# Kernel tuning notes

Hardware: AMD Instinct MI355X
Metric: run time of the kernel (lower is better)

## Reference

```python
import jax, jax.numpy as jnp
import numpy as np

FP8_MAX = 448.0  # max representable magnitude of float8_e4m3fn


def act_quant(x, block_size):
    """Blockwise fp8 quantization along the last dim.
    x: [M, K] -> q: [M, K//bs, bs] fp8, scale: [M, K//bs, 1] fp32."""
    m, k = x.shape
    xb = x.reshape(m, k // block_size, block_size)
    amax = jnp.max(jnp.abs(xb), axis=-1, keepdims=True)
    scale = jnp.maximum(amax, 1e-4) / FP8_MAX
    q = (xb / scale).astype(jnp.float8_e4m3fn)
    return q, scale


def dequant(q, scale):
    # q: [M, K//bs, bs], scale: [M, K//bs, 1] -> [M, K] fp32
    return (q.astype(jnp.float32) * scale).reshape(q.shape[0], -1)


def setup_inputs() -> dict:
    key = jax.random.key(0)
    k1, k2 = jax.random.split(key)
    B, S, D, F = 16, 4096, 512, 512
    x = jax.random.normal(k1, (B, S, D), dtype=jnp.float32)
    # lecun_normal-style init: std = 1/sqrt(fan_in)
    kernel = jax.random.normal(k2, (D, F), dtype=jnp.float32) / np.sqrt(D)
    bias = jnp.zeros((F,), dtype=jnp.float32)
    return {"x": x, "kernel": kernel, "bias": bias, "block_size": 128}


def reference(x, kernel, bias, block_size):
    input_shape = x.shape
    x_flat = x.reshape(-1, input_shape[-1])  # [M, K]
    # blockwise fp8 quantize activations and kernel
    xq, xs = act_quant(x_flat, block_size)
    kq, ks = act_quant(kernel, block_size)
    # fp8 GEMM with dequant scales == dequant-then-matmul in exact math
    y = dequant(xq, xs) @ dequant(kq, ks)  # [M, F]
    y = y + bias
    return y.reshape(input_shape[:-1] + (kernel.shape[1],))
```

## Files before the change

### kernel.cpp

```cpp
#include <hip/hip_runtime.h>
#include <hip/hip_bf16.h>

typedef __attribute__((ext_vector_type(4))) float  floatx4;
typedef __attribute__((ext_vector_type(2))) float  floatx2;
typedef __attribute__((ext_vector_type(8))) __bf16 bf16x8;

#define FP8_MAX 448.0f

__device__ __forceinline__ floatx2 fp8_qdq2(float a, float b) {
    int p = __builtin_amdgcn_cvt_pk_fp8_f32(a, b, 0, false);
    return __builtin_amdgcn_cvt_pk_f32_fp8(p, false);
}

__device__ __forceinline__ unsigned int f2bf(float f) {
    union { __hip_bfloat16 h; unsigned short u; } cv;
    cv.h = __float2bfloat16(f);
    return (unsigned int)cv.u;
}

__device__ __forceinline__ void async_copy16(void* lds, const void* g) {
    __builtin_amdgcn_global_load_lds(
        (const __attribute__((address_space(1))) unsigned int*)g,
        (__attribute__((address_space(3))) unsigned int*)lds,
        16, 0, 0);
}

__global__ void wdq_kernel(const float* __restrict__ W,
                           __hip_bfloat16* __restrict__ Wt) {
    const int D = 512, F = 512;
    int d = blockIdx.x;
    int t = threadIdx.x;
    float4 v = *reinterpret_cast<const float4*>(W + (size_t)d * F + t * 4);
    float am = fmaxf(fmaxf(fabsf(v.x), fabsf(v.y)), fmaxf(fabsf(v.z), fabsf(v.w)));
#pragma unroll
    for (int s = 16; s >= 1; s >>= 1) am = fmaxf(am, __shfl_xor(am, s));
    float scale = fmaxf(am, 1e-4f) / FP8_MAX;
    floatx2 d01 = fp8_qdq2(v.x / scale, v.y / scale);
    floatx2 d23 = fp8_qdq2(v.z / scale, v.w / scale);
    int f0 = t * 4;
    Wt[(size_t)(f0 + 0) * D + d] = __float2bfloat16(d01[0] * scale);
    Wt[(size_t)(f0 + 1) * D + d] = __float2bfloat16(d01[1] * scale);
    Wt[(size_t)(f0 + 2) * D + d] = __float2bfloat16(d23[0] * scale);
    Wt[(size_t)(f0 + 3) * D + d] = __float2bfloat16(d23[1] * scale);
}

#define BM 64
#define BN 256
#define BK 128

__global__ __launch_bounds__(256, 3) void fused_gemm(
        const float* __restrict__ X,
        const __hip_bfloat16* __restrict__ Wt,
        const float* __restrict__ bias,
        float* __restrict__ C, int M) {
    const int K = 512, N = 512;
    __shared__ __hip_bfloat16 As[BM][BK];
    __shared__ __hip_bfloat16 Bs[BN][64];

    int bx   = blockIdx.x;
    int tN   = bx & 1;
    int tM   = bx >> 1;
    int tid  = threadIdx.x;
    int wid  = tid >> 6;
    int lane = tid & 63;

    const float* Xb = X + (size_t)tM * BM * K;
    const __hip_bfloat16* Wb = Wt + (size_t)tN * BN * K;

    int ar = tid >> 2;
    int aq = tid & 3;

    floatx4 acc[4][4] = {};

    for (int kt = 0; kt < K / BK; ++kt) {
        const int k0 = kt * BK;

#pragma unroll
        for (int c = 0; c < 8; ++c) {
            int chunk = wid * 8 + c;
            int frow  = chunk * 8 + (lane >> 3);
            async_copy16((char*)&Bs[0][0] + chunk * 1024,
                         (const char*)(Wb + (size_t)frow * K + k0) + (lane & 7) * 16);
        }

        float4 v[8];
        const float* src = Xb + (size_t)ar * K + k0 + aq * 32;
#pragma unroll
        for (int j = 0; j < 8; ++j)
            v[j] = *reinterpret_cast<const float4*>(src + j * 4);
        float am = 0.f;
#pragma unroll
        for (int j = 0; j < 8; ++j)
            am = fmaxf(am, fmaxf(fmaxf(fabsf(v[j].x), fabsf(v[j].y)),
                                 fmaxf(fabsf(v[j].z), fabsf(v[j].w))));
        am = fmaxf(am, __shfl_xor(am, 1));
        am = fmaxf(am, __shfl_xor(am, 2));
        am = fmaxf(am, 1e-4f);
        float scale = am / FP8_MAX;
        float inv   = FP8_MAX / am;
        unsigned int* dst = (unsigned int*)&As[ar][aq * 32];
#pragma unroll
        for (int j = 0; j < 4; ++j) {
            floatx2 a0 = fp8_qdq2(v[2*j].x   * inv, v[2*j].y   * inv);
            floatx2 a1 = fp8_qdq2(v[2*j].z   * inv, v[2*j].w   * inv);
            floatx2 a2 = fp8_qdq2(v[2*j+1].x * inv, v[2*j+1].y * inv);
            floatx2 a3 = fp8_qdq2(v[2*j+1].z * inv, v[2*j+1].w * inv);
            uint4 o;
            o.x = f2bf(a0[0] * scale) | (f2bf(a0[1] * scale) << 16);
            o.y = f2bf(a1[0] * scale) | (f2bf(a1[1] * scale) << 16);
            o.z = f2bf(a2[0] * scale) | (f2bf(a2[1] * scale) << 16);
            o.w = f2bf(a3[0] * scale) | (f2bf(a3[1] * scale) << 16);
            *reinterpret_cast<uint4*>(dst + j * 4) = o;
        }
        __syncthreads();

#pragma unroll
        for (int h = 0; h < 2; ++h) {
            if (h) {
#pragma unroll
                for (int c = 0; c < 8; ++c) {
                    int chunk = wid * 8 + c;
                    int frow  = chunk * 8 + (lane >> 3);
                    async_copy16((char*)&Bs[0][0] + chunk * 1024,
                                 (const char*)(Wb + (size_t)frow * K + k0 + 64) + (lane & 7) * 16);
                }
                __syncthreads();
            }
#pragma unroll
            for (int ks = 0; ks < 2; ++ks) {
                int ksg = h * 2 + ks;
                bf16x8 a[4], b[4];
#pragma unroll
                for (int i = 0; i < 4; ++i) {
                    a[i] = *reinterpret_cast<const bf16x8*>(
                        &As[i * 16 + (lane & 15)][ksg * 32 + (lane >> 4) * 8]);
                    b[i] = *reinterpret_cast<const bf16x8*>(
                        &Bs[wid * 64 + i * 16 + (lane & 15)][ks * 32 + (lane >> 4) * 8]);
                }
#pragma unroll
                for (int mi = 0; mi < 4; ++mi)
#pragma unroll
                    for (int ni = 0; ni < 4; ++ni)
                        acc[mi][ni] = __builtin_amdgcn_mfma_f32_16x16x32_bf16(
                            a[mi], b[ni], acc[mi][ni], 0, 0, 0);
            }
            __syncthreads();
        }
    }

    int fcol = tN * BN + wid * 64 + (lane & 15);
    int mrow = tM * BM + ((lane >> 4) << 2);
#pragma unroll
    for (int ni = 0; ni < 4; ++ni) {
        int f = fcol + ni * 16;
        float bv = bias[f];
#pragma unroll
        for (int mi = 0; mi < 4; ++mi) {
            int m0 = mrow + mi * 16;
#pragma unroll
            for (int e = 0; e < 4; ++e)
                C[(size_t)(m0 + e) * N + f] = acc[mi][ni][e] + bv;
        }
    }
}

extern "C" void kernel_launch(void* const* d_in, const int* in_sizes, int n_in,
                              void* d_out, int out_size, void* d_ws, size_t ws_size,
                              hipStream_t stream) {
    const float* X    = (const float*)d_in[0];
    const float* W    = (const float*)d_in[1];
    const float* bias = (const float*)d_in[2];
    const int K = 512;
    const int M = in_sizes[0] / K;

    __hip_bfloat16* Wt = (__hip_bfloat16*)d_ws;

    wdq_kernel<<<dim3(512), dim3(128), 0, stream>>>(W, Wt);
    fused_gemm<<<dim3((M / BM) * (512 / BN)), dim3(256), 0, stream>>>(
        X, Wt, bias, (float*)d_out, M);
}
```

Measured before the change: 104.5 us.

## Double-buffer and software-pipeline fused quantize-GEMM with swizzled LDS and XCD remap

Restructures the fused quantize-GEMM into a double-buffered pipeline. It stages the next K-slice of W into LDS asynchronously while quantizing the next X block in registers and running MFMAs on the current buffers, with explicit waitcnt and barriers. The N tile shrinks from 256 to 128 with a 2x2 warp layout, LDS rows get an XOR swizzle to avoid bank conflicts, and tile indices are remapped so the four N tiles of an M tile land on the same XCD for L2 reuse of X. In exchange, each X row block is now read and re-quantized by four workgroups instead of two, which raises global and ALU traffic if L2 does not absorb it.

After: 111.7 us. 1.07x slower.

```diff
diff --git a/kernel.cpp b/kernel.cpp
--- a/kernel.cpp
+++ b/kernel.cpp
@@ -21,8 +21,7 @@
 __device__ __forceinline__ void async_copy16(void* lds, const void* g) {
     __builtin_amdgcn_global_load_lds(
         (const __attribute__((address_space(1))) unsigned int*)g,
-        (__attribute__((address_space(3))) unsigned int*)lds,
-        16, 0, 0);
+        (__attribute__((address_space(3))) unsigned int*)lds, 16, 0, 0);
 }
 
 __global__ void wdq_kernel(const float* __restrict__ W,
@@ -44,50 +43,38 @@
     Wt[(size_t)(f0 + 3) * D + d] = __float2bfloat16(d23[1] * scale);
 }
 
-#define BM 64
-#define BN 256
-#define BK 128
-
 __global__ __launch_bounds__(256, 3) void fused_gemm(
         const float* __restrict__ X,
         const __hip_bfloat16* __restrict__ Wt,
         const float* __restrict__ bias,
         float* __restrict__ C, int M) {
     const int K = 512, N = 512;
-    __shared__ __hip_bfloat16 As[BM][BK];
-    __shared__ __hip_bfloat16 Bs[BN][64];
-
-    int bx   = blockIdx.x;
-    int tN   = bx & 1;
-    int tM   = bx >> 1;
-    int tid  = threadIdx.x;
-    int wid  = tid >> 6;
-    int lane = tid & 63;
-
-    const float* Xb = X + (size_t)tM * BM * K;
-    const __hip_bfloat16* Wb = Wt + (size_t)tN * BN * K;
-
-    int ar = tid >> 2;
-    int aq = tid & 3;
-
-    floatx4 acc[4][4] = {};
-
-    for (int kt = 0; kt < K / BK; ++kt) {
-        const int k0 = kt * BK;
-
-#pragma unroll
-        for (int c = 0; c < 8; ++c) {
-            int chunk = wid * 8 + c;
-            int frow  = chunk * 8 + (lane >> 3);
-            async_copy16((char*)&Bs[0][0] + chunk * 1024,
-                         (const char*)(Wb + (size_t)frow * K + k0) + (lane & 7) * 16);
-        }
-
-        float4 v[8];
-        const float* src = Xb + (size_t)ar * K + k0 + aq * 32;
+    __shared__ char As[2][8192];
+    __shared__ char Bs[2][16384];
+
+    int bx = blockIdx.x, nwg = gridDim.x;
+    int tile = bx;
+    if ((nwg & 7) == 0) { int cpx = nwg >> 3; tile = (bx & 7) * cpx + (bx >> 3); }
+    int tN = tile & 3, tM = tile >> 2;
+
+    int tid = threadIdx.x, wid = tid >> 6, lane = tid & 63;
+    int wr = wid >> 1, wc = wid & 1;
+    int ar = tid >> 2, aq = tid & 3;
+
+    const float* Xb = X + (size_t)tM * 64 * K;
+    const __hip_bfloat16* Wb = Wt + (size_t)tN * 128 * K;
+
+    float4 v[8];
+    uint4  q4[4];
+    floatx4 acc[2][4] = {};
+
+    auto loadX = [&](int blk) {
+        const float* src = Xb + (size_t)ar * K + blk * 128 + aq * 32;
 #pragma unroll
         for (int j = 0; j < 8; ++j)
             v[j] = *reinterpret_cast<const float4*>(src + j * 4);
+    };
+    auto quantX = [&]() {
         float am = 0.f;
 #pragma unroll
         for (int j = 0; j < 8; ++j)
@@ -98,64 +85,112 @@
         am = fmaxf(am, 1e-4f);
         float scale = am / FP8_MAX;
         float inv   = FP8_MAX / am;
-        unsigned int* dst = (unsigned int*)&As[ar][aq * 32];
-#pragma unroll
-        for (int j = 0; j < 4; ++j) {
-            floatx2 a0 = fp8_qdq2(v[2*j].x   * inv, v[2*j].y   * inv);
-            floatx2 a1 = fp8_qdq2(v[2*j].z   * inv, v[2*j].w   * inv);
-            floatx2 a2 = fp8_qdq2(v[2*j+1].x * inv, v[2*j+1].y * inv);
-            floatx2 a3 = fp8_qdq2(v[2*j+1].z * inv, v[2*j+1].w * inv);
-            uint4 o;
-            o.x = f2bf(a0[0] * scale) | (f2bf(a0[1] * scale) << 16);
-            o.y = f2bf(a1[0] * scale) | (f2bf(a1[1] * scale) << 16);
-            o.z = f2bf(a2[0] * scale) | (f2bf(a2[1] * scale) << 16);
-            o.w = f2bf(a3[0] * scale) | (f2bf(a3[1] * scale) << 16);
-            *reinterpret_cast<uint4*>(dst + j * 4) = o;
-        }
-        __syncthreads();
-
-#pragma unroll
-        for (int h = 0; h < 2; ++h) {
-            if (h) {
-#pragma unroll
-                for (int c = 0; c < 8; ++c) {
-                    int chunk = wid * 8 + c;
-                    int frow  = chunk * 8 + (lane >> 3);
-                    async_copy16((char*)&Bs[0][0] + chunk * 1024,
-                                 (const char*)(Wb + (size_t)frow * K + k0 + 64) + (lane & 7) * 16);
-                }
-                __syncthreads();
+#pragma unroll
+        for (int n = 0; n < 4; ++n) {
+            floatx2 a0 = fp8_qdq2(v[2*n].x*inv,   v[2*n].y*inv);
+            floatx2 a1 = fp8_qdq2(v[2*n].z*inv,   v[2*n].w*inv);
+            floatx2 a2 = fp8_qdq2(v[2*n+1].x*inv, v[2*n+1].y*inv);
+            floatx2 a3 = fp8_qdq2(v[2*n+1].z*inv, v[2*n+1].w*inv);
+            q4[n].x = f2bf(a0[0]*scale) | (f2bf(a0[1]*scale) << 16);
+            q4[n].y = f2bf(a1[0]*scale) | (f2bf(a1[1]*scale) << 16);
+            q4[n].z = f2bf(a2[0]*scale) | (f2bf(a2[1]*scale) << 16);
+            q4[n].w = f2bf(a3[0]*scale) | (f2bf(a3[1]*scale) << 16);
+        }
+    };
+    auto stageB = [&](int buf, int k0) {
+#pragma unroll
+        for (int c = 0; c < 4; ++c) {
+            int chunk = wid * 4 + c;
+            int rr = chunk * 8 + (lane >> 3);
+            int s  = lane & 7;
+            const __hip_bfloat16* src =
+                Wb + (size_t)rr * K + k0 + ((s ^ (rr & 7)) << 3);
+            async_copy16(Bs[buf] + chunk * 1024, src);
+        }
+    };
+    auto writeA = [&](int buf, int hb) {
+        if ((aq >> 1) == hb) {
+            char* base = As[buf];
+#pragma unroll
+            for (int n = 0; n < 4; ++n) {
+                int slot = (aq & 1) * 4 + n;
+                *reinterpret_cast<uint4*>(
+                    base + ar * 128 + ((slot ^ (ar & 7)) << 4)) = q4[n];
             }
-#pragma unroll
-            for (int ks = 0; ks < 2; ++ks) {
-                int ksg = h * 2 + ks;
-                bf16x8 a[4], b[4];
-#pragma unroll
-                for (int i = 0; i < 4; ++i) {
-                    a[i] = *reinterpret_cast<const bf16x8*>(
-                        &As[i * 16 + (lane & 15)][ksg * 32 + (lane >> 4) * 8]);
-                    b[i] = *reinterpret_cast<const bf16x8*>(
-                        &Bs[wid * 64 + i * 16 + (lane & 15)][ks * 32 + (lane >> 4) * 8]);
-                }
-#pragma unroll
-                for (int mi = 0; mi < 4; ++mi)
-#pragma unroll
-                    for (int ni = 0; ni < 4; ++ni)
-                        acc[mi][ni] = __builtin_amdgcn_mfma_f32_16x16x32_bf16(
-                            a[mi], b[ni], acc[mi][ni], 0, 0, 0);
+        }
+    };
+    auto mfmaStep = [&](int buf) {
+        const char* ab = As[buf];
+        const char* bb = Bs[buf];
+#pragma unroll
+        for (int ks = 0; ks < 2; ++ks) {
+            int sl = ks * 4 + (lane >> 4);
+            bf16x8 a[2], b[4];
+#pragma unroll
+            for (int mi = 0; mi < 2; ++mi) {
+                int r = wr * 32 + mi * 16 + (lane & 15);
+                a[mi] = *reinterpret_cast<const bf16x8*>(
+                    ab + r * 128 + ((sl ^ (r & 7)) << 4));
             }
-            __syncthreads();
+#pragma unroll
+            for (int ni = 0; ni < 4; ++ni) {
+                int r = wc * 64 + ni * 16 + (lane & 15);
+                b[ni] = *reinterpret_cast<const bf16x8*>(
+                    bb + r * 128 + ((sl ^ (r & 7)) << 4));
+            }
+#pragma unroll
+            for (int mi = 0; mi < 2; ++mi)
+#pragma unroll
+                for (int ni = 0; ni < 4; ++ni)
+                    acc[mi][ni] = __builtin_amdgcn_mfma_f32_16x16x32_bf16(
+                        a[mi], b[ni], acc[mi][ni], 0, 0, 0);
+        }
+    };
+
+    loadX(0);
+    stageB(0, 0);
+    quantX();
+    loadX(1);
+    writeA(0, 0);
+    __syncthreads();
+
+#pragma unroll
+    for (int b = 0; b < 4; ++b) {
+        stageB(1, (2 * b + 1) * 64);
+        writeA(1, 1);
+        mfmaStep(0);
+        __builtin_amdgcn_sched_barrier(0);
+        asm volatile("s_waitcnt vmcnt(0) lgkmcnt(0)" ::: "memory");
+        __builtin_amdgcn_s_barrier();
+        __builtin_amdgcn_sched_barrier(0);
+
+        if (b < 3) {
+            stageB(0, (2 * b + 2) * 64);
+            quantX();
+            __builtin_amdgcn_sched_barrier(0);
+            if (b < 2) loadX(b + 2);
+            writeA(0, 0);
+            mfmaStep(1);
+            __builtin_amdgcn_sched_barrier(0);
+            if (b < 2)
+                asm volatile("s_waitcnt vmcnt(8) lgkmcnt(0)" ::: "memory");
+            else
+                asm volatile("s_waitcnt vmcnt(0) lgkmcnt(0)" ::: "memory");
+            __builtin_amdgcn_s_barrier();
+            __builtin_amdgcn_sched_barrier(0);
+        } else {
+            mfmaStep(1);
         }
     }
 
-    int fcol = tN * BN + wid * 64 + (lane & 15);
-    int mrow = tM * BM + ((lane >> 4) << 2);
+    int fcol = tN * 128 + wc * 64 + (lane & 15);
+    int mrow = tM * 64 + wr * 32 + ((lane >> 4) << 2);
 #pragma unroll
     for (int ni = 0; ni < 4; ++ni) {
         int f = fcol + ni * 16;
         float bv = bias[f];
 #pragma unroll
-        for (int mi = 0; mi < 4; ++mi) {
+        for (int mi = 0; mi < 2; ++mi) {
             int m0 = mrow + mi * 16;
 #pragma unroll
             for (int e = 0; e < 4; ++e)
@@ -176,6 +211,6 @@
     __hip_bfloat16* Wt = (__hip_bfloat16*)d_ws;
 
     wdq_kernel<<<dim3(512), dim3(128), 0, stream>>>(W, Wt);
-    fused_gemm<<<dim3((M / BM) * (512 / BN)), dim3(256), 0, stream>>>(
+    fused_gemm<<<dim3((M / 64) * (512 / 128)), dim3(256), 0, stream>>>(
         X, Wt, bias, (float*)d_out, M);
 }
```

## Restructure GEMM with register-resident A fragments, double-buffered swizzled B, XCD tile remap

Applied to the files above, without the earlier changes.

Tiles become 64x128 with a 2x2 warp layout. Each warp quantizes its A rows directly into MFMA register fragments, so the A shared-memory buffer and its round trip go away. The B tile is double-buffered in XOR-swizzled LDS and the next chunk is prefetched while MFMAs run on the current one. Blocks are remapped across the 8 XCDs for cache locality, and occupancy is raised to 4 blocks per SM. The cost is that each block now reads X twice (once per N half-pair), since X tiles are reused across 4 N-tiles instead of 2, and the dequant work is repeated per N-tile.

New measurement: 153.4 us. +46.8%, slower.

```diff
diff --git a/kernel.cpp b/kernel.cpp
--- a/kernel.cpp
+++ b/kernel.cpp
@@ -21,8 +21,7 @@
 __device__ __forceinline__ void async_copy16(void* lds, const void* g) {
     __builtin_amdgcn_global_load_lds(
         (const __attribute__((address_space(1))) unsigned int*)g,
-        (__attribute__((address_space(3))) unsigned int*)lds,
-        16, 0, 0);
+        (__attribute__((address_space(3))) unsigned int*)lds, 16, 0, 0);
 }
 
 __global__ void wdq_kernel(const float* __restrict__ W,
@@ -44,122 +43,123 @@
     Wt[(size_t)(f0 + 3) * D + d] = __float2bfloat16(d23[1] * scale);
 }
 
-#define BM 64
-#define BN 256
-#define BK 128
-
-__global__ __launch_bounds__(256, 3) void fused_gemm(
+__global__ __launch_bounds__(256, 4) void fused_gemm(
         const float* __restrict__ X,
         const __hip_bfloat16* __restrict__ Wt,
         const float* __restrict__ bias,
         float* __restrict__ C, int M) {
     const int K = 512, N = 512;
-    __shared__ __hip_bfloat16 As[BM][BK];
-    __shared__ __hip_bfloat16 Bs[BN][64];
+    __shared__ char Bs[2][16384];
 
     int bx   = blockIdx.x;
-    int tN   = bx & 1;
-    int tM   = bx >> 1;
-    int tid  = threadIdx.x;
-    int wid  = tid >> 6;
-    int lane = tid & 63;
+    int nwg  = gridDim.x;
+    int cpx  = nwg >> 3;
+    int tile = (bx & 7) * cpx + (bx >> 3);
+    int tN   = tile & 3;
+    int mg   = tile >> 2;
 
-    const float* Xb = X + (size_t)tM * BM * K;
-    const __hip_bfloat16* Wb = Wt + (size_t)tN * BN * K;
+    int tid = threadIdx.x, wid = tid >> 6, lane = tid & 63;
+    int wm = wid >> 1, wn = wid & 1;
+    int lr = lane & 15, lg = lane >> 4;
 
-    int ar = tid >> 2;
-    int aq = tid & 3;
+    const float* Xb = X + (size_t)(mg * 64) * K;
+    const __hip_bfloat16* Wb = Wt + (size_t)tN * 128 * K;
+    float* Cb = C + (size_t)(mg * 64) * N + tN * 128;
 
-    floatx4 acc[4][4] = {};
+    floatx4 acc[2][4] = {};
+    bf16x8  af[2][4];
 
-    for (int kt = 0; kt < K / BK; ++kt) {
-        const int k0 = kt * BK;
+    auto issueBs = [&](int buf, int step) {
+        const char* base = (const char*)Wb + step * 128;
+#pragma unroll
+        for (int cc = 0; cc < 4; ++cc) {
+            int c  = wid * 4 + cc;
+            int rr = c * 8 + (lane >> 3);
+            int d  = lane & 7;
+            async_copy16(Bs[buf] + c * 1024,
+                         base + (size_t)rr * (K * 2) + ((d ^ (rr & 7)) << 4));
+        }
+    };
+    auto quantA = [&](int kb) {
+#pragma unroll
+        for (int mi = 0; mi < 2; ++mi) {
+            const float* src = Xb + (size_t)(wm * 32 + mi * 16 + lr) * K
+                                  + kb * 128 + lg * 8;
+            float4 xv[8];
+#pragma unroll
+            for (int j = 0; j < 4; ++j) {
+                xv[2*j]   = *reinterpret_cast<const float4*>(src + 32 * j);
+                xv[2*j+1] = *reinterpret_cast<const float4*>(src + 32 * j + 4);
+            }
+            float am = 0.f;
+#pragma unroll
+            for (int j = 0; j < 8; ++j)
+                am = fmaxf(am, fmaxf(fmaxf(fabsf(xv[j].x), fabsf(xv[j].y)),
+                                     fmaxf(fabsf(xv[j].z), fabsf(xv[j].w))));
+            am = fmaxf(am, __shfl_xor(am, 16));
+            am = fmaxf(am, __shfl_xor(am, 32));
+            am = fmaxf(am, 1e-4f);
+            float scale = am / FP8_MAX;
+            float inv   = FP8_MAX / am;
+#pragma unroll
+            for (int j = 0; j < 4; ++j) {
+                floatx2 a0 = fp8_qdq2(xv[2*j].x*inv,   xv[2*j].y*inv);
+                floatx2 a1 = fp8_qdq2(xv[2*j].z*inv,   xv[2*j].w*inv);
+                floatx2 a2 = fp8_qdq2(xv[2*j+1].x*inv, xv[2*j+1].y*inv);
+                floatx2 a3 = fp8_qdq2(xv[2*j+1].z*inv, xv[2*j+1].w*inv);
+                uint4 o;
+                o.x = f2bf(a0[0]*scale) | (f2bf(a0[1]*scale) << 16);
+                o.y = f2bf(a1[0]*scale) | (f2bf(a1[1]*scale) << 16);
+                o.z = f2bf(a2[0]*scale) | (f2bf(a2[1]*scale) << 16);
+                o.w = f2bf(a3[0]*scale) | (f2bf(a3[1]*scale) << 16);
+                union { uint4 u; bf16x8 b; } cv; cv.u = o;
+                af[mi][j] = cv.b;
+            }
+        }
+    };
+    auto mfmaStep = [&](int buf, int h) {
+#pragma unroll
+        for (int ks = 0; ks < 2; ++ks) {
+            int sl = ks * 4 + lg;
+            bf16x8 b[4];
+#pragma unroll
+            for (int ni = 0; ni < 4; ++ni) {
+                int f = wn * 64 + ni * 16 + lr;
+                b[ni] = *reinterpret_cast<const bf16x8*>(
+                    Bs[buf] + f * 128 + ((sl ^ (f & 7)) << 4));
+            }
+#pragma unroll
+            for (int mi = 0; mi < 2; ++mi)
+#pragma unroll
+                for (int ni = 0; ni < 4; ++ni)
+                    acc[mi][ni] = __builtin_amdgcn_mfma_f32_16x16x32_bf16(
+                        af[mi][h * 2 + ks], b[ni], acc[mi][ni], 0, 0, 0);
+        }
+    };
+
+    issueBs(0, 0);
+    quantA(0);
+    __syncthreads();
 
 #pragma unroll
-        for (int c = 0; c < 8; ++c) {
-            int chunk = wid * 8 + c;
-            int frow  = chunk * 8 + (lane >> 3);
-            async_copy16((char*)&Bs[0][0] + chunk * 1024,
-                         (const char*)(Wb + (size_t)frow * K + k0) + (lane & 7) * 16);
-        }
-
-        float4 v[8];
-        const float* src = Xb + (size_t)ar * K + k0 + aq * 32;
-#pragma unroll
-        for (int j = 0; j < 8; ++j)
-            v[j] = *reinterpret_cast<const float4*>(src + j * 4);
-        float am = 0.f;
-#pragma unroll
-        for (int j = 0; j < 8; ++j)
-            am = fmaxf(am, fmaxf(fmaxf(fabsf(v[j].x), fabsf(v[j].y)),
-                                 fmaxf(fabsf(v[j].z), fabsf(v[j].w))));
-        am = fmaxf(am, __shfl_xor(am, 1));
-        am = fmaxf(am, __shfl_xor(am, 2));
-        am = fmaxf(am, 1e-4f);
-        float scale = am / FP8_MAX;
-        float inv   = FP8_MAX / am;
-        unsigned int* dst = (unsigned int*)&As[ar][aq * 32];
-#pragma unroll
-        for (int j = 0; j < 4; ++j) {
-            floatx2 a0 = fp8_qdq2(v[2*j].x   * inv, v[2*j].y   * inv);
-            floatx2 a1 = fp8_qdq2(v[2*j].z   * inv, v[2*j].w   * inv);
-            floatx2 a2 = fp8_qdq2(v[2*j+1].x * inv, v[2*j+1].y * inv);
-            floatx2 a3 = fp8_qdq2(v[2*j+1].z * inv, v[2*j+1].w * inv);
-            uint4 o;
-            o.x = f2bf(a0[0] * scale) | (f2bf(a0[1] * scale) << 16);
-            o.y = f2bf(a1[0] * scale) | (f2bf(a1[1] * scale) << 16);
-            o.z = f2bf(a2[0] * scale) | (f2bf(a2[1] * scale) << 16);
-            o.w = f2bf(a3[0] * scale) | (f2bf(a3[1] * scale) << 16);
-            *reinterpret_cast<uint4*>(dst + j * 4) = o;
-        }
-        __syncthreads();
+    for (int s = 0; s < 8; ++s) {
+        int cur = s & 1, nxt = cur ^ 1;
+        if (s < 7) issueBs(nxt, s + 1);
+        if (s && (s & 1) == 0) quantA(s >> 1);
+        mfmaStep(cur, s & 1);
+        if (s < 7) __syncthreads();
+    }
 
 #pragma unroll
-        for (int h = 0; h < 2; ++h) {
-            if (h) {
+    for (int ni = 0; ni < 4; ++ni) {
+        int col = wn * 64 + ni * 16 + lr;
+        float bv = bias[tN * 128 + col];
 #pragma unroll
-                for (int c = 0; c < 8; ++c) {
-                    int chunk = wid * 8 + c;
-                    int frow  = chunk * 8 + (lane >> 3);
-                    async_copy16((char*)&Bs[0][0] + chunk * 1024,
-                                 (const char*)(Wb + (size_t)frow * K + k0 + 64) + (lane & 7) * 16);
-                }
-                __syncthreads();
-            }
-#pragma unroll
-            for (int ks = 0; ks < 2; ++ks) {
-                int ksg = h * 2 + ks;
-                bf16x8 a[4], b[4];
-#pragma unroll
-                for (int i = 0; i < 4; ++i) {
-                    a[i] = *reinterpret_cast<const bf16x8*>(
-                        &As[i * 16 + (lane & 15)][ksg * 32 + (lane >> 4) * 8]);
-                    b[i] = *reinterpret_cast<const bf16x8*>(
-                        &Bs[wid * 64 + i * 16 + (lane & 15)][ks * 32 + (lane >> 4) * 8]);
-                }
-#pragma unroll
-                for (int mi = 0; mi < 4; ++mi)
-#pragma unroll
-                    for (int ni = 0; ni < 4; ++ni)
-                        acc[mi][ni] = __builtin_amdgcn_mfma_f32_16x16x32_bf16(
-                            a[mi], b[ni], acc[mi][ni], 0, 0, 0);
-            }
-            __syncthreads();
-        }
-    }
-
-    int fcol = tN * BN + wid * 64 + (lane & 15);
-    int mrow = tM * BM + ((lane >> 4) << 2);
-#pragma unroll
-    for (int ni = 0; ni < 4; ++ni) {
-        int f = fcol + ni * 16;
-        float bv = bias[f];
-#pragma unroll
-        for (int mi = 0; mi < 4; ++mi) {
-            int m0 = mrow + mi * 16;
+        for (int mi = 0; mi < 2; ++mi) {
+            int r0 = wm * 32 + mi * 16 + lg * 4;
 #pragma unroll
             for (int e = 0; e < 4; ++e)
-                C[(size_t)(m0 + e) * N + f] = acc[mi][ni][e] + bv;
+                Cb[(size_t)(r0 + e) * N + col] = acc[mi][ni][e] + bv;
         }
     }
 }
@@ -176,6 +176,6 @@
     __hip_bfloat16* Wt = (__hip_bfloat16*)d_ws;
 
     wdq_kernel<<<dim3(512), dim3(128), 0, stream>>>(W, Wt);
-    fused_gemm<<<dim3((M / BM) * (512 / BN)), dim3(256), 0, stream>>>(
+    fused_gemm<<<dim3((M / 64) * 4), dim3(256), 0, stream>>>(
         X, Wt, bias, (float*)d_out, M);
 }
```

## Split X quant into separate kernel and triple-buffer async GEMM with swizzled LDS

Applied to the files above, without the earlier changes.

Moves activation fp8 quantize-dequantize out of the GEMM into a standalone kernel that writes a bf16 copy of X to workspace. The GEMM then loads both operands with async global-to-LDS copies into a 3-stage ring buffer using XOR-swizzled layout, with 128x256 tiles, 8 waves, and a tile-order remap. The intent is to overlap loads with MFMA and avoid bank conflicts. The cost is an extra full write and read of the bf16 activations (about 64MB more traffic) plus an extra kernel launch.

Result: faster. 99.38 us (-4.9%).

```diff
diff --git a/kernel.cpp b/kernel.cpp
--- a/kernel.cpp
+++ b/kernel.cpp
@@ -21,8 +21,7 @@
 __device__ __forceinline__ void async_copy16(void* lds, const void* g) {
     __builtin_amdgcn_global_load_lds(
         (const __attribute__((address_space(1))) unsigned int*)g,
-        (__attribute__((address_space(3))) unsigned int*)lds,
-        16, 0, 0);
+        (__attribute__((address_space(3))) unsigned int*)lds, 16, 0, 0);
 }
 
 __global__ void wdq_kernel(const float* __restrict__ W,
@@ -44,122 +43,129 @@
     Wt[(size_t)(f0 + 3) * D + d] = __float2bfloat16(d23[1] * scale);
 }
 
-#define BM 64
-#define BN 256
-#define BK 128
+__global__ void xqdq_kernel(const float* __restrict__ X,
+                            __hip_bfloat16* __restrict__ Xdq) {
+    int tid = threadIdx.x;
+    size_t row = (size_t)blockIdx.x * 2 + (tid >> 7);
+    int cg = tid & 127;
+    const float4 v = *reinterpret_cast<const float4*>(X + row * 512 + cg * 4);
+    float am = fmaxf(fmaxf(fabsf(v.x), fabsf(v.y)), fmaxf(fabsf(v.z), fabsf(v.w)));
+    am = fmaxf(am, __shfl_xor(am, 1));
+    am = fmaxf(am, __shfl_xor(am, 2));
+    am = fmaxf(am, __shfl_xor(am, 4));
+    am = fmaxf(am, __shfl_xor(am, 8));
+    am = fmaxf(am, __shfl_xor(am, 16));
+    am = fmaxf(am, 1e-4f);
+    float scale = am / FP8_MAX;
+    float inv   = FP8_MAX / am;
+    floatx2 d01 = fp8_qdq2(v.x * inv, v.y * inv);
+    floatx2 d23 = fp8_qdq2(v.z * inv, v.w * inv);
+    uint2 o;
+    o.x = f2bf(d01[0] * scale) | (f2bf(d01[1] * scale) << 16);
+    o.y = f2bf(d23[0] * scale) | (f2bf(d23[1] * scale) << 16);
+    *reinterpret_cast<uint2*>(Xdq + row * 512 + cg * 4) = o;
+}
 
-__global__ __launch_bounds__(256, 3) void fused_gemm(
-        const float* __restrict__ X,
+__global__ __launch_bounds__(512, 1) void gemm8(
+        const __hip_bfloat16* __restrict__ Xdq,
         const __hip_bfloat16* __restrict__ Wt,
         const float* __restrict__ bias,
         float* __restrict__ C, int M) {
     const int K = 512, N = 512;
-    __shared__ __hip_bfloat16 As[BM][BK];
-    __shared__ __hip_bfloat16 Bs[BN][64];
+    __shared__ char lds[3][49152];
 
     int bx   = blockIdx.x;
-    int tN   = bx & 1;
-    int tM   = bx >> 1;
-    int tid  = threadIdx.x;
-    int wid  = tid >> 6;
-    int lane = tid & 63;
+    int tile = (bx & 7) * (gridDim.x >> 3) + (bx >> 3);
+    int tn   = tile & 1;
+    int tm   = tile >> 1;
 
-    const float* Xb = X + (size_t)tM * BM * K;
-    const __hip_bfloat16* Wb = Wt + (size_t)tN * BN * K;
+    int tid = threadIdx.x, wid = tid >> 6, lane = tid & 63;
+    int wm = wid >> 2, wn = wid & 3;
+    int lr = lane & 15, lg = lane >> 4;
 
-    int ar = tid >> 2;
-    int aq = tid & 3;
+    const char* Abase = (const char*)(Xdq + (size_t)tm * 128 * K);
+    const char* Bbase = (const char*)(Wt + (size_t)tn * 256 * K);
+    float* Cb = C + (size_t)tm * 128 * N + tn * 256;
 
     floatx4 acc[4][4] = {};
 
-    for (int kt = 0; kt < K / BK; ++kt) {
-        const int k0 = kt * BK;
+    auto stage = [&](int buf, int t) {
+        int kb = t * 128;
+#pragma unroll
+        for (int i = 0; i < 2; ++i) {
+            int c = wid * 2 + i;
+            int r = c * 8 + (lane >> 3);
+            int s = lane & 7;
+            async_copy16(lds[buf] + c * 1024,
+                         Abase + (size_t)r * 1024 + kb + ((s ^ (r & 7)) << 4));
+        }
+#pragma unroll
+        for (int i = 0; i < 4; ++i) {
+            int c = wid * 4 + i;
+            int f = c * 8 + (lane >> 3);
+            int s = lane & 7;
+            async_copy16(lds[buf] + 16384 + c * 1024,
+                         Bbase + (size_t)f * 1024 + kb + ((s ^ (f & 7)) << 4));
+        }
+    };
+
+    float bv[4];
+#pragma unroll
+    for (int ni = 0; ni < 4; ++ni)
+        bv[ni] = bias[tn * 256 + wn * 64 + ni * 16 + lr];
+    stage(0, 0);
+    stage(1, 1);
+    asm volatile("s_waitcnt vmcnt(6)" ::: "memory");
+    __builtin_amdgcn_s_barrier();
+    __builtin_amdgcn_sched_barrier(0);
 
 #pragma unroll
-        for (int c = 0; c < 8; ++c) {
-            int chunk = wid * 8 + c;
-            int frow  = chunk * 8 + (lane >> 3);
-            async_copy16((char*)&Bs[0][0] + chunk * 1024,
-                         (const char*)(Wb + (size_t)frow * K + k0) + (lane & 7) * 16);
-        }
-
-        float4 v[8];
-        const float* src = Xb + (size_t)ar * K + k0 + aq * 32;
+    for (int t = 0; t < 8; ++t) {
+        const char* Ab = lds[t % 3];
+        const char* Bb = lds[t % 3] + 16384;
+        if (t < 6) stage((t + 2) % 3, t + 2);
+        __builtin_amdgcn_s_setprio(1);
 #pragma unroll
-        for (int j = 0; j < 8; ++j)
-            v[j] = *reinterpret_cast<const float4*>(src + j * 4);
-        float am = 0.f;
+        for (int ks = 0; ks < 2; ++ks) {
+            int q = (ks << 2) | lg;
+            bf16x8 a[4], b[4];
 #pragma unroll
-        for (int j = 0; j < 8; ++j)
-            am = fmaxf(am, fmaxf(fmaxf(fabsf(v[j].x), fabsf(v[j].y)),
-                                 fmaxf(fabsf(v[j].z), fabsf(v[j].w))));
-        am = fmaxf(am, __shfl_xor(am, 1));
-        am = fmaxf(am, __shfl_xor(am, 2));
-        am = fmaxf(am, 1e-4f);
-        float scale = am / FP8_MAX;
-        float inv   = FP8_MAX / am;
-        unsigned int* dst = (unsigned int*)&As[ar][aq * 32];
-#pragma unroll
-        for (int j = 0; j < 4; ++j) {
-            floatx2 a0 = fp8_qdq2(v[2*j].x   * inv, v[2*j].y   * inv);
-            floatx2 a1 = fp8_qdq2(v[2*j].z   * inv, v[2*j].w   * inv);
-            floatx2 a2 = fp8_qdq2(v[2*j+1].x * inv, v[2*j+1].y * inv);
-            floatx2 a3 = fp8_qdq2(v[2*j+1].z * inv, v[2*j+1].w * inv);
-            uint4 o;
-            o.x = f2bf(a0[0] * scale) | (f2bf(a0[1] * scale) << 16);
-            o.y = f2bf(a1[0] * scale) | (f2bf(a1[1] * scale) << 16);
-            o.z = f2bf(a2[0] * scale) | (f2bf(a2[1] * scale) << 16);
-            o.w = f2bf(a3[0] * scale) | (f2bf(a3[1] * scale) << 16);
-            *reinterpret_cast<uint4*>(dst + j * 4) = o;
-        }
-        __syncthreads();
-
-#pragma unroll
-        for (int h = 0; h < 2; ++h) {
-            if (h) {
-#pragma unroll
-                for (int c = 0; c < 8; ++c) {
-                    int chunk = wid * 8 + c;
-                    int frow  = chunk * 8 + (lane >> 3);
-                    async_copy16((char*)&Bs[0][0] + chunk * 1024,
-                                 (const char*)(Wb + (size_t)frow * K + k0 + 64) + (lane & 7) * 16);
-                }
-                __syncthreads();
+            for (int mi = 0; mi < 4; ++mi) {
+                int r = wm * 64 + mi * 16 + lr;
+                a[mi] = *reinterpret_cast<const bf16x8*>(
+                    Ab + r * 128 + ((q ^ (r & 7)) << 4));
             }
 #pragma unroll
-            for (int ks = 0; ks < 2; ++ks) {
-                int ksg = h * 2 + ks;
-                bf16x8 a[4], b[4];
+            for (int ni = 0; ni < 4; ++ni) {
+                int f = wn * 64 + ni * 16 + lr;
+                b[ni] = *reinterpret_cast<const bf16x8*>(
+                    Bb + f * 128 + ((q ^ (f & 7)) << 4));
+            }
 #pragma unroll
-                for (int i = 0; i < 4; ++i) {
-                    a[i] = *reinterpret_cast<const bf16x8*>(
-                        &As[i * 16 + (lane & 15)][ksg * 32 + (lane >> 4) * 8]);
-                    b[i] = *reinterpret_cast<const bf16x8*>(
-                        &Bs[wid * 64 + i * 16 + (lane & 15)][ks * 32 + (lane >> 4) * 8]);
-                }
+            for (int mi = 0; mi < 4; ++mi)
 #pragma unroll
-                for (int mi = 0; mi < 4; ++mi)
-#pragma unroll
-                    for (int ni = 0; ni < 4; ++ni)
-                        acc[mi][ni] = __builtin_amdgcn_mfma_f32_16x16x32_bf16(
-                            a[mi], b[ni], acc[mi][ni], 0, 0, 0);
-            }
-            __syncthreads();
+                for (int ni = 0; ni < 4; ++ni)
+                    acc[mi][ni] = __builtin_amdgcn_mfma_f32_16x16x32_bf16(
+                        a[mi], b[ni], acc[mi][ni], 0, 0, 0);
+        }
+        __builtin_amdgcn_s_setprio(0);
+        if (t < 7) {
+            if (t < 6) asm volatile("s_waitcnt vmcnt(6)" ::: "memory");
+            else       asm volatile("s_waitcnt vmcnt(0)" ::: "memory");
+            __builtin_amdgcn_s_barrier();
+            __builtin_amdgcn_sched_barrier(0);
         }
     }
 
-    int fcol = tN * BN + wid * 64 + (lane & 15);
-    int mrow = tM * BM + ((lane >> 4) << 2);
 #pragma unroll
     for (int ni = 0; ni < 4; ++ni) {
-        int f = fcol + ni * 16;
-        float bv = bias[f];
+        int col = wn * 64 + ni * 16 + lr;
 #pragma unroll
         for (int mi = 0; mi < 4; ++mi) {
-            int m0 = mrow + mi * 16;
+            int r0 = wm * 64 + mi * 16 + lg * 4;
 #pragma unroll
             for (int e = 0; e < 4; ++e)
-                C[(size_t)(m0 + e) * N + f] = acc[mi][ni][e] + bv;
+                Cb[(size_t)(r0 + e) * N + col] = acc[mi][ni][e] + bv[ni];
         }
     }
 }
@@ -173,9 +179,11 @@
     const int K = 512;
     const int M = in_sizes[0] / K;
 
-    __hip_bfloat16* Wt = (__hip_bfloat16*)d_ws;
+    __hip_bfloat16* Wt  = (__hip_bfloat16*)d_ws;
+    __hip_bfloat16* Xdq = Wt + 512 * 512;
 
     wdq_kernel<<<dim3(512), dim3(128), 0, stream>>>(W, Wt);
-    fused_gemm<<<dim3((M / BM) * (512 / BN)), dim3(256), 0, stream>>>(
-        X, Wt, bias, (float*)d_out, M);
+    xqdq_kernel<<<dim3(M / 2), dim3(256), 0, stream>>>(X, Xdq);
+    gemm8<<<dim3((M / 128) * 2), dim3(512), 0, stream>>>(
+        Xdq, Wt, bias, (float*)d_out, M);
 }
```
